# Kernel optimization log

Hardware: AMD Instinct MI355X
Metric: run time of the kernel (lower is better)

## Reference

```python
import jax, jax.numpy as jnp
import numpy as np

KERNEL = 3  # kernel_size from init_kwargs


def _unfold(x, k):
    """torch.nn.functional.unfold with padding=k//2, stride=1.
    Returns [b, c*k*k, h*w] with torch's ordering: index = c*(k*k) + kh*k + kw.
    """
    b, c, h, w = x.shape
    p = k // 2
    xp = jnp.pad(x, ((0, 0), (0, 0), (p, p), (p, p)))
    # fixed k*k = 9 slices (small static loop, not a data-dim loop)
    cols = jnp.stack(
        [xp[:, :, i:i + h, j:j + w] for i in range(k) for j in range(k)],
        axis=2,
    )  # [b, c, k*k, h, w]
    return cols.reshape(b, c * k * k, h * w)


def setup_inputs() -> dict:
    key = jax.random.key(0)
    k1, k2 = jax.random.split(key)
    x = jax.random.normal(k1, (8, 64, 128, 128), dtype=jnp.float32)
    # memory parameter: torch.rand -> uniform [0, 1), shape [c*k*k, out_channels]
    memory = jax.random.uniform(k2, (64 * KERNEL * KERNEL, 128), dtype=jnp.float32)
    return {"x": x, "memory": memory}


def reference(x, memory):
    b, c, h, w = x.shape
    cols = _unfold(x, KERNEL)                 # [b, c*k*k, h*w]
    cols = jax.nn.softmax(cols, axis=1)       # softmax over unfolded patch dim
    out = jnp.einsum('ki,bkl->bil', memory, cols)  # [b, out_ch, h*w]
    return out.reshape(b, memory.shape[1], h, w)
```

## Files before the change

### kernel.cpp

```cpp
#include <hip/hip_runtime.h>
#include <stdint.h>


#define Cn 64
#define Hn 128
#define Wn 128
#define OC 128
#define HW (Hn * Wn)

typedef __attribute__((ext_vector_type(8))) short bf16x8_t;
typedef __attribute__((ext_vector_type(4))) float f32x4_t;
typedef __attribute__((ext_vector_type(16))) float f32x16_t;

__device__ inline unsigned short f2bf(float f) {
    union { float f; uint32_t u; } v; v.f = f;
    uint32_t u = v.u;
    u += 0x7fffu + ((u >> 16) & 1u);
    return (unsigned short)(u >> 16);
}
__device__ inline float bf_lo(uint32_t u) {
    union { uint32_t u; float f; } v; v.u = u << 16;
    return v.f;
}
__device__ inline float bf_hi(uint32_t u) {
    union { uint32_t u; float f; } v; v.u = u & 0xffff0000u;
    return v.f;
}

__global__ void prep_b2(const float* __restrict__ mem, uint4* __restrict__ Bt2,
                        uint4* __restrict__ ones) {
    if (blockIdx.x == 36) {
        if (threadIdx.x < 8)
            ones[threadIdx.x] = make_uint4(0x3F803F80u, 0x3F803F80u, 0x3F803F80u, 0x3F803F80u);
        return;
    }
    int u = blockIdx.x * 256 + threadIdx.x;
    int n = u & 127;
    int cid = u >> 7;
    int hi = cid & 1;
    int kc = cid >> 1;
    int q = kc >> 2, cblk = kc & 3;
    unsigned short h8[8];
#pragma unroll
    for (int j = 0; j < 8; j++) {
        int c = cblk * 16 + hi * 8 + j;
        h8[j] = f2bf(mem[(c * 9 + q) * OC + n]);
    }
    Bt2[cid * 128 + n] = *(const uint4*)h8;
}

__global__ __launch_bounds__(256) void exp_tr4(const float* __restrict__ x,
                                               uint4* __restrict__ Etu,
                                               float* __restrict__ S) {
    __shared__ uint32_t L[32 * 132];
    __shared__ float Spart[512];
    int bid = blockIdx.x;
    int b = bid >> 7, h = bid & 127;
    int t = threadIdx.x;
    int wv = t >> 6, lane = t & 63;

    const float* xr = x + (size_t)b * Cn * HW + h * Wn;
    float s0 = 0.f, s1 = 0.f;
#pragma unroll
    for (int i = 0; i < 8; i++) {
        int cp = wv * 8 + i;
        const float* r0 = xr + (size_t)(2 * cp) * HW + 2 * lane;
        float2 v0 = *(const float2*)r0;
        float2 v1 = *(const float2*)(r0 + HW);
        uint32_t p0 = (uint32_t)f2bf(__expf(v0.x)) | ((uint32_t)f2bf(__expf(v1.x)) << 16);
        uint32_t p1 = (uint32_t)f2bf(__expf(v0.y)) | ((uint32_t)f2bf(__expf(v1.y)) << 16);
        s0 += bf_lo(p0) + bf_hi(p0);
        s1 += bf_lo(p1) + bf_hi(p1);
        *(uint2*)&L[cp * 132 + 2 * lane] = make_uint2(p0, p1);
    }
    *(float2*)&Spart[wv * 128 + 2 * lane] = make_float2(s0, s1);
    __syncthreads();

    int w = t >> 1, half = t & 1;
    uint32_t us[16];
#pragma unroll
    for (int j = 0; j < 16; j++)
        us[j] = L[(half * 16 + j) * 132 + w];
    size_t pix = (size_t)(b * Hn + h) * Wn + w;
    uint4* dst = Etu + pix * 8 + half * 4;
    const uint4* sv = (const uint4*)us;
    dst[0] = sv[0]; dst[1] = sv[1]; dst[2] = sv[2]; dst[3] = sv[3];

    if (half == 0)
        S[pix] = Spart[w] + Spart[128 + w] + Spart[256 + w] + Spart[384 + w];
}

__global__ __launch_bounds__(256, 2) void conv4(const uint4* __restrict__ Etu,
                                                const uint4* __restrict__ Bt2,
                                                const float* __restrict__ S,
                                                const uint4* __restrict__ ones,
                                                float* __restrict__ out) {
    __shared__ __align__(16) uint4 EtL[324 * 8];
    __shared__ float Sh[324];
    __shared__ float Zt[256];

    int bid = blockIdx.x;
    int b = bid >> 6;
    int ty = (bid >> 3) & 7, tx = bid & 7;
    int h0 = ty * 16, w0 = tx * 16;
    int t = threadIdx.x;

    const uint4* Etb = Etu + (size_t)b * HW * 8;
#pragma unroll
    for (int i = 0; i < 11; i++) {
        int qd = i * 256 + t;
        if (qd < 2592) {
            int p = qd >> 3, slot = qd & 7;
            int py = p / 18, px = p - py * 18;
            int gy = h0 - 1 + py, gx = w0 - 1 + px;
            bool in = (gy >= 0) & (gy < Hn) & (gx >= 0) & (gx < Wn);
            int g = slot ^ (p & 7);
            const uint4* src = in ? (Etb + ((size_t)(gy * Wn + gx)) * 8 + g)
                                  : (ones + g);
            EtL[p * 8 + slot] = *src;
        }
    }
#pragma unroll
    for (int i = 0; i < 2; i++) {
        int p = i * 256 + t;
        if (p < 324) {
            int py = p / 18, px = p - py * 18;
            int gy = h0 - 1 + py, gx = w0 - 1 + px;
            bool in = (gy >= 0) & (gy < Hn) & (gx >= 0) & (gx < Wn);
            Sh[p] = in ? S[(size_t)b * HW + gy * Wn + gx] : 64.0f;
        }
    }
    __syncthreads();

    {
        int zy = t >> 4, zx = t & 15;
        float z = 0.f;
#pragma unroll
        for (int dy = 0; dy < 3; dy++)
#pragma unroll
            for (int dx = 0; dx < 3; dx++)
                z += Sh[(zy + dy) * 18 + (zx + dx)];
        Zt[t] = 1.0f / z;
    }
    __syncthreads();

    int lane = t & 63, wv = t >> 6;
    int l31 = lane & 31, hi = lane >> 5;
    int x0v = l31 & 15;
    int y0[2];
    y0[0] = (wv * 2 + 0) * 2 + (l31 >> 4);
    y0[1] = (wv * 2 + 1) * 2 + (l31 >> 4);

    f32x16_t acc[2][4];
#pragma unroll
    for (int j = 0; j < 2; j++)
#pragma unroll
        for (int g = 0; g < 4; g++)
#pragma unroll
            for (int r = 0; r < 16; r++) acc[j][g][r] = 0.f;

    bf16x8_t Wf[3][4], Ef[3][2];

    auto loadW = [&](int kc, int s) {
        const uint4* bp = Bt2 + (size_t)((kc * 2 + hi) * 128 + l31);
#pragma unroll
        for (int g = 0; g < 4; g++)
            Wf[s][g] = *(const bf16x8_t*)(bp + g * 32);
    };
    auto loadE = [&](int kc, int s) {
        int q = kc >> 2, cblk = kc & 3;
        int kh = q / 3, kw = q - kh * 3;
        int g = cblk * 2 + hi;
#pragma unroll
        for (int j = 0; j < 2; j++) {
            int pix = (y0[j] + kh) * 18 + (x0v + kw);
            Ef[s][j] = *(const bf16x8_t*)&EtL[pix * 8 + (g ^ (pix & 7))];
        }
    };

    loadW(0, 0); loadE(0, 0);
    loadW(1, 1); loadE(1, 1);
    loadW(2, 2); loadE(2, 2);
#pragma unroll
    for (int kc = 0; kc < 36; kc++) {
        int s = kc % 3;
#pragma unroll
        for (int g = 0; g < 4; g++)
#pragma unroll
            for (int j = 0; j < 2; j++)
                acc[j][g] = __builtin_amdgcn_mfma_f32_32x32x16_bf16(
                    Wf[s][g], Ef[s][j], acc[j][g], 0, 0, 0);
        if (kc + 3 < 36) { loadW(kc + 3, s); loadE(kc + 3, s); }
    }

#pragma unroll
    for (int j = 0; j < 2; j++) {
        float zi = Zt[(wv * 2 + j) * 32 + l31];
        float* ob = out + (size_t)b * OC * HW + (h0 + y0[j]) * Wn + (w0 + x0v)
                  + (size_t)(4 * hi) * HW;
#pragma unroll
        for (int g = 0; g < 4; g++) {
#pragma unroll
            for (int r = 0; r < 16; r++) {
                int nrel = g * 32 + (r & 3) + 8 * (r >> 2);
                ob[(size_t)nrel * HW] = acc[j][g][r] * zi;
            }
        }
    }
}

extern "C" void kernel_launch(void* const* d_in, const int* in_sizes, int n_in,
                              void* d_out, int out_size, void* d_ws, size_t ws_size,
                              hipStream_t stream) {
    const float* x = (const float*)d_in[0];
    const float* mem = (const float*)d_in[1];
    float* out = (float*)d_out;
    char* ws = (char*)d_ws;

    uint4* Etu = (uint4*)ws;
    float* S = (float*)(ws + 16777216);
    uint4* Bt2 = (uint4*)(ws + 17301504);
    uint4* ones = (uint4*)(ws + 17448960);

    prep_b2<<<37, 256, 0, stream>>>(mem, Bt2, ones);
    exp_tr4<<<1024, 256, 0, stream>>>(x, Etu, S);
    conv4<<<512, 256, 0, stream>>>(Etu, Bt2, S, ones, out);
}
```

Measured before the change: 115.7 us.

## Fuse exp/transpose stage into conv kernel, computing patch sums in-tile

Removes the separate exp_tr4 kernel and its intermediate bf16 workspace. The conv kernel now reads fp32 x directly, applies exp, packs to bf16 into the swizzled LDS tile including halo, and computes per-pixel channel sums from LDS. This drops a global write/read round trip of about 16 MB and one launch. In exchange, halo pixels get their exp recomputed, and the tile load uses strided per-channel global reads.

```diff
diff --git a/kernel.cpp b/kernel.cpp
--- a/kernel.cpp
+++ b/kernel.cpp
@@ -9,7 +9,6 @@
 #define HW (Hn * Wn)
 
 typedef __attribute__((ext_vector_type(8))) short bf16x8_t;
-typedef __attribute__((ext_vector_type(4))) float f32x4_t;
 typedef __attribute__((ext_vector_type(16))) float f32x16_t;
 
 __device__ inline unsigned short f2bf(float f) {
@@ -27,13 +26,7 @@
     return v.f;
 }
 
-__global__ void prep_b2(const float* __restrict__ mem, uint4* __restrict__ Bt2,
-                        uint4* __restrict__ ones) {
-    if (blockIdx.x == 36) {
-        if (threadIdx.x < 8)
-            ones[threadIdx.x] = make_uint4(0x3F803F80u, 0x3F803F80u, 0x3F803F80u, 0x3F803F80u);
-        return;
-    }
+__global__ void prep_b2(const float* __restrict__ mem, uint4* __restrict__ Bt2) {
     int u = blockIdx.x * 256 + threadIdx.x;
     int n = u & 127;
     int cid = u >> 7;
@@ -49,51 +42,8 @@
     Bt2[cid * 128 + n] = *(const uint4*)h8;
 }
 
-__global__ __launch_bounds__(256) void exp_tr4(const float* __restrict__ x,
-                                               uint4* __restrict__ Etu,
-                                               float* __restrict__ S) {
-    __shared__ uint32_t L[32 * 132];
-    __shared__ float Spart[512];
-    int bid = blockIdx.x;
-    int b = bid >> 7, h = bid & 127;
-    int t = threadIdx.x;
-    int wv = t >> 6, lane = t & 63;
-
-    const float* xr = x + (size_t)b * Cn * HW + h * Wn;
-    float s0 = 0.f, s1 = 0.f;
-#pragma unroll
-    for (int i = 0; i < 8; i++) {
-        int cp = wv * 8 + i;
-        const float* r0 = xr + (size_t)(2 * cp) * HW + 2 * lane;
-        float2 v0 = *(const float2*)r0;
-        float2 v1 = *(const float2*)(r0 + HW);
-        uint32_t p0 = (uint32_t)f2bf(__expf(v0.x)) | ((uint32_t)f2bf(__expf(v1.x)) << 16);
-        uint32_t p1 = (uint32_t)f2bf(__expf(v0.y)) | ((uint32_t)f2bf(__expf(v1.y)) << 16);
-        s0 += bf_lo(p0) + bf_hi(p0);
-        s1 += bf_lo(p1) + bf_hi(p1);
-        *(uint2*)&L[cp * 132 + 2 * lane] = make_uint2(p0, p1);
-    }
-    *(float2*)&Spart[wv * 128 + 2 * lane] = make_float2(s0, s1);
-    __syncthreads();
-
-    int w = t >> 1, half = t & 1;
-    uint32_t us[16];
-#pragma unroll
-    for (int j = 0; j < 16; j++)
-        us[j] = L[(half * 16 + j) * 132 + w];
-    size_t pix = (size_t)(b * Hn + h) * Wn + w;
-    uint4* dst = Etu + pix * 8 + half * 4;
-    const uint4* sv = (const uint4*)us;
-    dst[0] = sv[0]; dst[1] = sv[1]; dst[2] = sv[2]; dst[3] = sv[3];
-
-    if (half == 0)
-        S[pix] = Spart[w] + Spart[128 + w] + Spart[256 + w] + Spart[384 + w];
-}
-
-__global__ __launch_bounds__(256, 2) void conv4(const uint4* __restrict__ Etu,
+__global__ __launch_bounds__(256, 2) void convf(const float* __restrict__ x,
                                                 const uint4* __restrict__ Bt2,
-                                                const float* __restrict__ S,
-                                                const uint4* __restrict__ ones,
                                                 float* __restrict__ out) {
     __shared__ __align__(16) uint4 EtL[324 * 8];
     __shared__ float Sh[324];
@@ -104,30 +54,74 @@
     int ty = (bid >> 3) & 7, tx = bid & 7;
     int h0 = ty * 16, w0 = tx * 16;
     int t = threadIdx.x;
-
-    const uint4* Etb = Etu + (size_t)b * HW * 8;
-#pragma unroll
-    for (int i = 0; i < 11; i++) {
-        int qd = i * 256 + t;
-        if (qd < 2592) {
-            int p = qd >> 3, slot = qd & 7;
-            int py = p / 18, px = p - py * 18;
-            int gy = h0 - 1 + py, gx = w0 - 1 + px;
-            bool in = (gy >= 0) & (gy < Hn) & (gx >= 0) & (gx < Wn);
-            int g = slot ^ (p & 7);
-            const uint4* src = in ? (Etb + ((size_t)(gy * Wn + gx)) * 8 + g)
-                                  : (ones + g);
-            EtL[p * 8 + slot] = *src;
-        }
-    }
-#pragma unroll
-    for (int i = 0; i < 2; i++) {
-        int p = i * 256 + t;
+    uint32_t* Lu = (uint32_t*)EtL;
+
+    const float* xb = x + (size_t)b * Cn * HW;
+
+#pragma unroll
+    for (int i = 0; i < 9; i++) {
+        int u = i * 256 + t;
+        int qx = u & 3;
+        int w2 = u >> 2;
+        int py = w2 % 18;
+        int cp = w2 / 18;
+        int gy = h0 - 1 + py;
+        int g = cp >> 2, jj = cp & 3;
+        int pb = py * 18 + 1 + qx * 4;
+        uint32_t pk0, pk1, pk2, pk3;
+        if (gy >= 0 && gy < Hn) {
+            const float* r0 = xb + (size_t)(2 * cp) * HW + gy * Wn + w0 + qx * 4;
+            float4 v0 = *(const float4*)r0;
+            float4 v1 = *(const float4*)(r0 + HW);
+            pk0 = (uint32_t)f2bf(__expf(v0.x)) | ((uint32_t)f2bf(__expf(v1.x)) << 16);
+            pk1 = (uint32_t)f2bf(__expf(v0.y)) | ((uint32_t)f2bf(__expf(v1.y)) << 16);
+            pk2 = (uint32_t)f2bf(__expf(v0.z)) | ((uint32_t)f2bf(__expf(v1.z)) << 16);
+            pk3 = (uint32_t)f2bf(__expf(v0.w)) | ((uint32_t)f2bf(__expf(v1.w)) << 16);
+        } else {
+            pk0 = pk1 = pk2 = pk3 = 0x3F803F80u;
+        }
+        Lu[(pb + 0) * 32 + (((g ^ ((pb + 0) & 7)) << 2) | jj)] = pk0;
+        Lu[(pb + 1) * 32 + (((g ^ ((pb + 1) & 7)) << 2) | jj)] = pk1;
+        Lu[(pb + 2) * 32 + (((g ^ ((pb + 2) & 7)) << 2) | jj)] = pk2;
+        Lu[(pb + 3) * 32 + (((g ^ ((pb + 3) & 7)) << 2) | jj)] = pk3;
+    }
+
+#pragma unroll
+    for (int i = 0; i < 5; i++) {
+        int u = i * 256 + t;
+        if (u < 1152) {
+            int side = u & 1;
+            int v = u >> 1;
+            int py = v % 18;
+            int cp = v / 18;
+            int gy = h0 - 1 + py;
+            int gx = side ? (w0 + 16) : (w0 - 1);
+            int p = py * 18 + side * 17;
+            int g = cp >> 2, jj = cp & 3;
+            uint32_t pk;
+            if (gy >= 0 && gy < Hn && gx >= 0 && gx < Wn) {
+                const float* r0 = xb + (size_t)(2 * cp) * HW + gy * Wn + gx;
+                pk = (uint32_t)f2bf(__expf(r0[0])) | ((uint32_t)f2bf(__expf(r0[HW])) << 16);
+            } else {
+                pk = 0x3F803F80u;
+            }
+            Lu[p * 32 + (((g ^ (p & 7)) << 2) | jj)] = pk;
+        }
+    }
+    __syncthreads();
+
+#pragma unroll
+    for (int pi = 0; pi < 2; pi++) {
+        int p = pi * 256 + t;
         if (p < 324) {
-            int py = p / 18, px = p - py * 18;
-            int gy = h0 - 1 + py, gx = w0 - 1 + px;
-            bool in = (gy >= 0) & (gy < Hn) & (gx >= 0) & (gx < Wn);
-            Sh[p] = in ? S[(size_t)b * HW + gy * Wn + gx] : 64.0f;
+            float s = 0.f;
+#pragma unroll
+            for (int k = 0; k < 8; k++) {
+                uint4 q = EtL[p * 8 + ((k + t) & 7)];
+                s += bf_lo(q.x) + bf_hi(q.x) + bf_lo(q.y) + bf_hi(q.y)
+                   + bf_lo(q.z) + bf_hi(q.z) + bf_lo(q.w) + bf_hi(q.w);
+            }
+            Sh[p] = s;
         }
     }
     __syncthreads();
@@ -215,14 +209,9 @@
     const float* x = (const float*)d_in[0];
     const float* mem = (const float*)d_in[1];
     float* out = (float*)d_out;
-    char* ws = (char*)d_ws;
-
-    uint4* Etu = (uint4*)ws;
-    float* S = (float*)(ws + 16777216);
-    uint4* Bt2 = (uint4*)(ws + 17301504);
-    uint4* ones = (uint4*)(ws + 17448960);
-
-    prep_b2<<<37, 256, 0, stream>>>(mem, Bt2, ones);
-    exp_tr4<<<1024, 256, 0, stream>>>(x, Etu, S);
-    conv4<<<512, 256, 0, stream>>>(Etu, Bt2, S, ones, out);
-}
+
+    uint4* Bt2 = (uint4*)d_ws;
+
+    prep_b2<<<36, 256, 0, stream>>>(mem, Bt2);
+    convf<<<512, 256, 0, stream>>>(x, Bt2, out);
+}
```

Result: slower. 121.9 us (+5.3%).

## Split conv output channels across waves with smaller 8x16 tiles

Applied to the files above, without the earlier changes.

The conv kernel now uses 512-thread blocks over 8x16 pixel tiles, and each of 8 waves computes 32 output channels for 32 pixel pairs instead of all 128 channels. This reduces per-thread accumulators from 128 to 32 floats to raise occupancy, and remaps block IDs to interleave batches. The normaliser is computed per-lane inline, which removes one barrier. In exchange, halo overhead per tile grows and each wave repeats the E fragment reads from LDS. The LDS swizzle is also changed to reduce bank conflicts.

```diff
diff --git a/kernel.cpp b/kernel.cpp
--- a/kernel.cpp
+++ b/kernel.cpp
@@ -9,7 +9,6 @@
 #define HW (Hn * Wn)
 
 typedef __attribute__((ext_vector_type(8))) short bf16x8_t;
-typedef __attribute__((ext_vector_type(4))) float f32x4_t;
 typedef __attribute__((ext_vector_type(16))) float f32x16_t;
 
 __device__ inline unsigned short f2bf(float f) {
@@ -90,91 +89,77 @@
         S[pix] = Spart[w] + Spart[128 + w] + Spart[256 + w] + Spart[384 + w];
 }
 
-__global__ __launch_bounds__(256, 2) void conv4(const uint4* __restrict__ Etu,
+__global__ __launch_bounds__(512, 4) void convf(const uint4* __restrict__ Etu,
                                                 const uint4* __restrict__ Bt2,
                                                 const float* __restrict__ S,
                                                 const uint4* __restrict__ ones,
                                                 float* __restrict__ out) {
-    __shared__ __align__(16) uint4 EtL[324 * 8];
-    __shared__ float Sh[324];
-    __shared__ float Zt[256];
-
-    int bid = blockIdx.x;
-    int b = bid >> 6;
-    int ty = (bid >> 3) & 7, tx = bid & 7;
-    int h0 = ty * 16, w0 = tx * 16;
+    __shared__ __align__(16) uint4 EtL[184 * 8];
+    __shared__ float Sh[184];
+
+    int bid0 = blockIdx.x;
+    int bid = ((bid0 & 7) << 7) | (bid0 >> 3);
+    int b = bid >> 7;
+    int ty = (bid >> 3) & 15, tx = bid & 7;
+    int h0 = ty * 8, w0 = tx * 16;
     int t = threadIdx.x;
+    int lane = t & 63, wv = t >> 6;
 
     const uint4* Etb = Etu + (size_t)b * HW * 8;
-#pragma unroll
-    for (int i = 0; i < 11; i++) {
-        int qd = i * 256 + t;
-        if (qd < 2592) {
-            int p = qd >> 3, slot = qd & 7;
-            int py = p / 18, px = p - py * 18;
-            int gy = h0 - 1 + py, gx = w0 - 1 + px;
-            bool in = (gy >= 0) & (gy < Hn) & (gx >= 0) & (gx < Wn);
-            int g = slot ^ (p & 7);
-            const uint4* src = in ? (Etb + ((size_t)(gy * Wn + gx)) * 8 + g)
-                                  : (ones + g);
-            EtL[p * 8 + slot] = *src;
+
+    {
+        int pr = lane >> 3, slot = lane & 7;
+#pragma unroll
+        for (int i = 0; i < 3; i++) {
+            int grp = wv + 8 * i;
+            if (grp < 23) {
+                int p = grp * 8 + pr;
+                int py = p / 18, px = p - py * 18;
+                int gy = h0 - 1 + py, gx = w0 - 1 + px;
+                bool in = (p < 180) & (gy >= 0) & (gy < Hn) & (gx >= 0) & (gx < Wn);
+                int g = slot ^ ((p >> 1) & 7);
+                const uint4* src = in ? (Etb + ((size_t)(gy * Wn + gx)) * 8 + g)
+                                      : (ones + g);
+                EtL[p * 8 + slot] = *src;
+            }
         }
     }
-#pragma unroll
-    for (int i = 0; i < 2; i++) {
-        int p = i * 256 + t;
-        if (p < 324) {
-            int py = p / 18, px = p - py * 18;
-            int gy = h0 - 1 + py, gx = w0 - 1 + px;
-            bool in = (gy >= 0) & (gy < Hn) & (gx >= 0) & (gx < Wn);
-            Sh[p] = in ? S[(size_t)b * HW + gy * Wn + gx] : 64.0f;
-        }
+    if (t < 184) {
+        int py = t / 18, px = t - py * 18;
+        int gy = h0 - 1 + py, gx = w0 - 1 + px;
+        bool in = (t < 180) & (gy >= 0) & (gy < Hn) & (gx >= 0) & (gx < Wn);
+        Sh[t] = in ? S[(size_t)b * HW + gy * Wn + gx] : 64.0f;
     }
     __syncthreads();
 
-    {
-        int zy = t >> 4, zx = t & 15;
-        float z = 0.f;
-#pragma unroll
-        for (int dy = 0; dy < 3; dy++)
-#pragma unroll
-            for (int dx = 0; dx < 3; dx++)
-                z += Sh[(zy + dy) * 18 + (zx + dx)];
-        Zt[t] = 1.0f / z;
-    }
-    __syncthreads();
-
-    int lane = t & 63, wv = t >> 6;
+    int wid = wv;
+    int wo = wid & 3;
+    int wp = wid >> 2;
     int l31 = lane & 31, hi = lane >> 5;
     int x0v = l31 & 15;
     int y0[2];
-    y0[0] = (wv * 2 + 0) * 2 + (l31 >> 4);
-    y0[1] = (wv * 2 + 1) * 2 + (l31 >> 4);
-
-    f32x16_t acc[2][4];
+    y0[0] = (wp * 2 + 0) * 2 + (l31 >> 4);
+    y0[1] = (wp * 2 + 1) * 2 + (l31 >> 4);
+
+    f32x16_t acc[2];
 #pragma unroll
     for (int j = 0; j < 2; j++)
 #pragma unroll
-        for (int g = 0; g < 4; g++)
-#pragma unroll
-            for (int r = 0; r < 16; r++) acc[j][g][r] = 0.f;
-
-    bf16x8_t Wf[3][4], Ef[3][2];
+        for (int r = 0; r < 16; r++) acc[j][r] = 0.f;
+
+    bf16x8_t Wf[3], Ef[3][2];
 
     auto loadW = [&](int kc, int s) {
-        const uint4* bp = Bt2 + (size_t)((kc * 2 + hi) * 128 + l31);
-#pragma unroll
-        for (int g = 0; g < 4; g++)
-            Wf[s][g] = *(const bf16x8_t*)(bp + g * 32);
+        Wf[s] = *(const bf16x8_t*)(Bt2 + (size_t)((kc * 2 + hi) * 128 + wo * 32 + l31));
     };
     auto loadE = [&](int kc, int s) {
         int q = kc >> 2, cblk = kc & 3;
         int kh = q / 3, kw = q - kh * 3;
-        int g = cblk * 2 + hi;
+        int ge = cblk * 2 + hi;
 #pragma unroll
         for (int j = 0; j < 2; j++) {
             int pix = (y0[j] + kh) * 18 + (x0v + kw);
-            Ef[s][j] = *(const bf16x8_t*)&EtL[pix * 8 + (g ^ (pix & 7))];
+            Ef[s][j] = *(const bf16x8_t*)&EtL[pix * 8 + (ge ^ ((pix >> 1) & 7))];
         }
     };
 
@@ -185,26 +170,27 @@
     for (int kc = 0; kc < 36; kc++) {
         int s = kc % 3;
 #pragma unroll
-        for (int g = 0; g < 4; g++)
-#pragma unroll
-            for (int j = 0; j < 2; j++)
-                acc[j][g] = __builtin_amdgcn_mfma_f32_32x32x16_bf16(
-                    Wf[s][g], Ef[s][j], acc[j][g], 0, 0, 0);
+        for (int j = 0; j < 2; j++)
+            acc[j] = __builtin_amdgcn_mfma_f32_32x32x16_bf16(
+                Wf[s], Ef[s][j], acc[j], 0, 0, 0);
         if (kc + 3 < 36) { loadW(kc + 3, s); loadE(kc + 3, s); }
     }
 
 #pragma unroll
     for (int j = 0; j < 2; j++) {
-        float zi = Zt[(wv * 2 + j) * 32 + l31];
-        float* ob = out + (size_t)b * OC * HW + (h0 + y0[j]) * Wn + (w0 + x0v)
-                  + (size_t)(4 * hi) * HW;
-#pragma unroll
-        for (int g = 0; g < 4; g++) {
-#pragma unroll
-            for (int r = 0; r < 16; r++) {
-                int nrel = g * 32 + (r & 3) + 8 * (r >> 2);
-                ob[(size_t)nrel * HW] = acc[j][g][r] * zi;
-            }
+        float z = 0.f;
+#pragma unroll
+        for (int dy = 0; dy < 3; dy++)
+#pragma unroll
+            for (int dx = 0; dx < 3; dx++)
+                z += Sh[(y0[j] + dy) * 18 + (x0v + dx)];
+        float zi = 1.0f / z;
+        float* ob = out + (size_t)b * OC * HW + (size_t)(wo * 32 + 4 * hi) * HW
+                  + (h0 + y0[j]) * Wn + (w0 + x0v);
+#pragma unroll
+        for (int r = 0; r < 16; r++) {
+            int nrel = (r & 3) + 8 * (r >> 2);
+            ob[(size_t)nrel * HW] = acc[j][r] * zi;
         }
     }
 }
@@ -224,5 +210,5 @@
 
     prep_b2<<<37, 256, 0, stream>>>(mem, Bt2, ones);
     exp_tr4<<<1024, 256, 0, stream>>>(x, Etu, S);
-    conv4<<<512, 256, 0, stream>>>(Etu, Bt2, S, ones, out);
-}
+    convf<<<1024, 512, 0, stream>>>(Etu, Bt2, S, ones, out);
+}
```

Result: no change. 115.0 us (-0.6%).
